# Kernel tuning notes

Measured on AMD Instinct MI355X. Metric: run time of the kernel, lower is better.

## Reference

```python
import jax, jax.numpy as jnp
import numpy as np

B, N, C = 4, 2048, 768
H = 12
DH = C // H
HID = int(C * 4.0)
SCALE = DH ** -0.5
EPS = 1e-5


def layernorm(x, g, b):
    mu = jnp.mean(x, axis=-1, keepdims=True)
    var = jnp.var(x, axis=-1, keepdims=True)
    return (x - mu) * jax.lax.rsqrt(var + EPS) * g + b


def setup_inputs() -> dict:
    key = jax.random.key(0)
    ks = jax.random.split(key, 10)
    s = lambda fan_in: 1.0 / np.sqrt(fan_in)
    return {
        "x": jax.random.normal(ks[0], (B, N, C), dtype=jnp.float32),
        "ln1_g": jnp.ones((C,), jnp.float32),
        "ln1_b": jnp.zeros((C,), jnp.float32),
        "w_qkv": jax.random.uniform(ks[1], (C, 3 * C), jnp.float32, -s(C), s(C)),
        "w_proj": jax.random.uniform(ks[2], (C, C), jnp.float32, -s(C), s(C)),
        "b_proj": jnp.zeros((C,), jnp.float32),
        "ln2_g": jnp.ones((C,), jnp.float32),
        "ln2_b": jnp.zeros((C,), jnp.float32),
        "w_fc1": jax.random.uniform(ks[3], (C, HID), jnp.float32, -s(C), s(C)),
        "b_fc1": jnp.zeros((HID,), jnp.float32),
        "w_fc2": jax.random.uniform(ks[4], (HID, C), jnp.float32, -s(HID), s(HID)),
        "b_fc2": jnp.zeros((C,), jnp.float32),
    }


def reference(x, ln1_g, ln1_b, w_qkv, w_proj, b_proj, ln2_g, ln2_b, w_fc1, b_fc1, w_fc2, b_fc2):
    # --- attention branch ---
    h = layernorm(x, ln1_g, ln1_b)                       # [B,N,C]
    qkv = (h @ w_qkv).reshape(B, N, 3, H, DH)
    q = qkv[:, :, 0].transpose(0, 2, 1, 3)               # [B,H,N,DH]
    k = qkv[:, :, 1].transpose(0, 2, 1, 3)
    v = qkv[:, :, 2].transpose(0, 2, 1, 3)
    attn = jnp.einsum('bhnd,bhmd->bhnm', q, k) * SCALE   # [B,H,N,N]
    attn = jax.nn.softmax(attn, axis=-1)
    y = jnp.einsum('bhnm,bhmd->bhnd', attn, v)           # [B,H,N,DH]
    y = y.transpose(0, 2, 1, 3).reshape(B, N, C)
    y = y @ w_proj + b_proj
    x = x + y
    # --- MLP branch ---
    h = layernorm(x, ln2_g, ln2_b)
    h = jax.nn.gelu(h @ w_fc1 + b_fc1, approximate=False)
    h = h @ w_fc2 + b_fc2
    return x + h
```

## Files before the change

kernel.cpp:

```cpp
#include <hip/hip_runtime.h>
#include <stdint.h>

#define DEV __device__ __forceinline__

typedef __attribute__((ext_vector_type(8))) short bf16x8;
typedef __attribute__((ext_vector_type(4))) float f32x4;
typedef __attribute__((ext_vector_type(4))) short s16x4;

DEV short f2bf(float f) {
    union { float f; unsigned u; } v; v.f = f;
    unsigned r = v.u + 0x7fffu + ((v.u >> 16) & 1u);
    return (short)(r >> 16);
}

DEV uint32_t cvtpk(float lo, float hi) {
    uint32_t r;
    asm("v_cvt_pk_bf16_f32 %0, %1, %2" : "=v"(r) : "v"(lo), "v"(hi));
    return r;
}

typedef const unsigned int __attribute__((address_space(1)))* gp1;
typedef unsigned int __attribute__((address_space(3)))* lp3;

DEV void gload16(const void* g, void* l) {
    __builtin_amdgcn_global_load_lds((gp1)g, (lp3)l, 16, 0, 0);
}

DEV void wait1_barrier() { asm volatile("s_waitcnt vmcnt(1)\ns_barrier" ::: "memory"); }
DEV void wait0_barrier() { asm volatile("s_waitcnt vmcnt(0)\ns_barrier" ::: "memory"); }

__global__ __launch_bounds__(256) void tcvt4(
    const float* __restrict__ W0, short* __restrict__ T0,
    const float* __restrict__ W1, short* __restrict__ T1,
    const float* __restrict__ W2, short* __restrict__ T2,
    const float* __restrict__ W3, short* __restrict__ T3)
{
    __shared__ float t[32][33];
    int bid = blockIdx.x;
    const float* W; short* WT; int K, N, nx, lb;
    if (bid < 1728)      { W = W0; WT = T0; K = 768;  N = 2304; nx = 72; lb = bid; }
    else if (bid < 2304) { W = W1; WT = T1; K = 768;  N = 768;  nx = 24; lb = bid - 1728; }
    else if (bid < 4608) { W = W2; WT = T2; K = 768;  N = 3072; nx = 96; lb = bid - 2304; }
    else                 { W = W3; WT = T3; K = 3072; N = 768;  nx = 24; lb = bid - 4608; }
    int n0 = (lb % nx) * 32, k0 = (lb / nx) * 32;
    int tx = threadIdx.x & 31, ty = threadIdx.x >> 5;
#pragma unroll
    for (int i = 0; i < 32; i += 8)
        t[ty + i][tx] = W[(size_t)(k0 + ty + i) * N + n0 + tx];
    __syncthreads();
#pragma unroll
    for (int i = 0; i < 32; i += 8)
        WT[(size_t)(n0 + ty + i) * K + k0 + tx] = f2bf(t[tx][ty + i]);
}

__global__ __launch_bounds__(256) void ln_bf16(
    const float* __restrict__ x, const float* __restrict__ gam,
    const float* __restrict__ bet, short* __restrict__ out)
{
    const int w = threadIdx.x >> 6, lane = threadIdx.x & 63;
    const size_t row = (size_t)blockIdx.x * 4 + w;
    const float* xr = x + row * 768;
    float4 v[3];
    float s = 0.f, ss = 0.f;
#pragma unroll
    for (int k = 0; k < 3; ++k) {
        v[k] = *(const float4*)(xr + k * 256 + lane * 4);
        s  += v[k].x + v[k].y + v[k].z + v[k].w;
        ss += v[k].x * v[k].x + v[k].y * v[k].y + v[k].z * v[k].z + v[k].w * v[k].w;
    }
#pragma unroll
    for (int i = 1; i < 64; i <<= 1) { s += __shfl_xor(s, i, 64); ss += __shfl_xor(ss, i, 64); }
    const float inv = 1.f / 768.f;
    float mu = s * inv;
    float var = ss * inv - mu * mu;
    float rstd = rsqrtf(var + 1e-5f);
#pragma unroll
    for (int k = 0; k < 3; ++k) {
        int c = k * 256 + lane * 4;
        float vv[4] = { v[k].x, v[k].y, v[k].z, v[k].w };
        s16x4 o;
#pragma unroll
        for (int j = 0; j < 4; ++j)
            o[j] = f2bf((vv[j] - mu) * rstd * gam[c + j] + bet[c + j]);
        *(s16x4*)(out + row * 768 + c) = o;
    }
}

template<int MODE>
DEV void gemm_body(
    const short* __restrict__ A, const short* __restrict__ Bt,
    int M, int N, int K,
    const float* __restrict__ bias, const float* __restrict__ resid,
    float* __restrict__ outf, short* __restrict__ outb,
    short* __restrict__ qo, short* __restrict__ ko, short* __restrict__ vo,
    char* lds)
{
    const int tid = threadIdx.x;
    const int w = tid >> 6, lane = tid & 63;
    const int g = lane >> 4, l15 = lane & 15;
    const int brow = blockIdx.x * 128, bcol = blockIdx.y * 128;
    const int wr = w >> 2, wc = w & 3;
    f32x4 acc[2][2] = {};

    int aoff[2], boff[2];
#pragma unroll
    for (int m = 0; m < 2; ++m) {
        int ra = wr * 32 + m * 16 + l15;
        aoff[m] = ra * 64 + ((g * 16) ^ (((ra >> 1) & 3) << 4));
    }
#pragma unroll
    for (int n = 0; n < 2; ++n) {
        int rb = wc * 32 + n * 16 + l15;
        boff[n] = 8192 + rb * 64 + ((g * 16) ^ (((rb >> 1) & 3) << 4));
    }
    const int dStage = tid * 16;
    const char* pSrc;
    {
        int r = dStage >> 6, b = dStage & 63;
        int bs = b ^ (((r >> 1) & 3) << 4);
        pSrc = (tid < 512)
             ? (const char*)(A  + (size_t)(brow + r) * K) + bs
             : (const char*)(Bt + (size_t)(bcol + (r - 128)) * K) + bs;
    }

#define GSTAGE(BUF, OFF) gload16(pSrc + (OFF), lds + (BUF) * 16384 + dStage)

    const int KT = K >> 5;
    GSTAGE(0, 0);
    GSTAGE(1, 64);
    wait1_barrier();

    const int NM = KT / 3;
    for (int mi = 0; mi < NM; ++mi) {
#pragma unroll
        for (int u = 0; u < 3; ++u) {
            const int s = mi * 3 + u;
            if (s + 2 < KT) GSTAGE((u + 2) % 3, (u + 2) * 64);
            bf16x8 af[2], bfg[2];
#pragma unroll
            for (int m = 0; m < 2; ++m)
                af[m]  = *(const bf16x8*)(lds + u * 16384 + aoff[m]);
#pragma unroll
            for (int n = 0; n < 2; ++n)
                bfg[n] = *(const bf16x8*)(lds + u * 16384 + boff[n]);
#pragma unroll
            for (int m = 0; m < 2; ++m)
#pragma unroll
                for (int n = 0; n < 2; ++n)
                    acc[m][n] = __builtin_amdgcn_mfma_f32_16x16x32_bf16(af[m], bfg[n], acc[m][n], 0, 0, 0);
            if (s + 1 < KT) {
                if (s + 2 < KT) wait1_barrier();
                else            wait0_barrier();
            }
        }
        pSrc += 192;
    }
#undef GSTAGE

#pragma unroll
    for (int m = 0; m < 2; ++m) {
#pragma unroll
        for (int n = 0; n < 2; ++n) {
#pragma unroll
            for (int j = 0; j < 4; ++j) {
                int r = brow + wr * 32 + m * 16 + g * 4 + j;
                int c = bcol + wc * 32 + n * 16 + l15;
                float v = acc[m][n][j];
                if (MODE == 0) {
                    int which = c / 768, cc = c % 768;
                    int h = cc >> 6, d = cc & 63;
                    int b_ = r >> 11, nn = r & 2047;
                    size_t bh = (size_t)b_ * 12 + h;
                    if (which == 0)      qo[(bh * 2048 + nn) * 64 + d] = f2bf(v * 0.18033688011112042f);
                    else if (which == 1) ko[(bh * 2048 + nn) * 64 + d] = f2bf(v);
                    else                 vo[(bh * 64 + d) * 2048 + nn] = f2bf(v);
                } else if (MODE == 1) {
                    outf[(size_t)r * N + c] = v + bias[c] + resid[(size_t)r * N + c];
                } else {
                    float t = v + bias[c];
                    float ge = 0.5f * t * (1.0f + erff(t * 0.70710678118654752f));
                    outb[(size_t)r * N + c] = f2bf(ge);
                }
            }
        }
    }
}

__global__ __launch_bounds__(1024, 8) void g_qkv(
    const short* A, const short* Bt, int M, int N, int K,
    short* qo, short* ko, short* vo)
{
    __shared__ __align__(16) char lds[49152];
    gemm_body<0>(A, Bt, M, N, K, nullptr, nullptr, nullptr, nullptr, qo, ko, vo, lds);
}
__global__ __launch_bounds__(1024, 8) void g_proj(
    const short* A, const short* Bt, int M, int N, int K,
    const float* bias, const float* resid, float* outf)
{
    __shared__ __align__(16) char lds[49152];
    gemm_body<1>(A, Bt, M, N, K, bias, resid, outf, nullptr, nullptr, nullptr, nullptr, lds);
}
__global__ __launch_bounds__(1024, 8) void g_fc1(
    const short* A, const short* Bt, int M, int N, int K,
    const float* bias, short* outb)
{
    __shared__ __align__(16) char lds[49152];
    gemm_body<2>(A, Bt, M, N, K, bias, nullptr, nullptr, outb, nullptr, nullptr, nullptr, lds);
}
__global__ __launch_bounds__(1024, 8) void g_fc2(
    const short* A, const short* Bt, int M, int N, int K,
    const float* bias, const float* resid, float* outf)
{
    __shared__ __align__(16) char lds[49152];
    gemm_body<1>(A, Bt, M, N, K, bias, resid, outf, nullptr, nullptr, nullptr, nullptr, lds);
}

__global__ __launch_bounds__(256, 3) void attn_fwd(
    const short* __restrict__ Q, const short* __restrict__ Kg,
    const short* __restrict__ Vt, short* __restrict__ Y)
{
    __shared__ __align__(16) char alds[43008];
    const int tid = threadIdx.x, w = tid >> 6, lane = tid & 63;
    const int g = lane >> 4, l15 = lane & 15;
    const int bid = blockIdx.y * gridDim.x + blockIdx.x;
    const int nwg = gridDim.x * gridDim.y;
    const int logical = (bid & 7) * (nwg >> 3) + (bid >> 3);
    const int bh = logical >> 4;
    const int q0 = (logical & 15) * 128 + w * 32;
    const short* Qb = Q  + (size_t)bh * 2048 * 64;
    const short* Kb = Kg + (size_t)bh * 2048 * 64;
    const short* Vb = Vt + (size_t)bh * 64 * 2048;

    bf16x8 qf[2][2];
#pragma unroll
    for (int m = 0; m < 2; ++m)
#pragma unroll
        for (int kk = 0; kk < 2; ++kk)
            qf[m][kk] = *(const bf16x8*)(Qb + (size_t)(q0 + m * 16 + l15) * 64 + kk * 32 + g * 8);

    f32x4 accO[2][4] = {};
    float lpart[2] = { 0.f, 0.f };

    int koff[2][2], voff[4], poff[2], pwoff[2][2];
#pragma unroll
    for (int n = 0; n < 2; ++n) {
        int key = n * 16 + l15;
#pragma unroll
        for (int kk = 0; kk < 2; ++kk)
            koff[kk][n] = key * 128 + ((kk * 64 + g * 16) ^ ((key & 7) << 4));
    }
#pragma unroll
    for (int n = 0; n < 4; ++n) {
        int d = n * 16 + l15;
        voff[n] = 16384 + d * 64 + ((g * 16) ^ (((d >> 1) & 3) << 4));
    }
#pragma unroll
    for (int m = 0; m < 2; ++m) {
        int qr = m * 16 + l15;
        poff[m] = 32768 + w * 2560 + qr * 80 + g * 16;
#pragma unroll
        for (int n = 0; n < 2; ++n)
            pwoff[m][n] = 32768 + w * 2560 + qr * 80 + n * 32 + g * 8;
    }
    int dK, dV; const char* pK3; const char* pV3;
    {
        int bb = w * 1024;
        int L = bb + lane * 16;
        int rk = L >> 7, bk_ = L & 127;
        int bsk = bk_ ^ ((rk & 7) << 4);
        dK = bb;
        pK3 = (const char*)(Kb + (size_t)rk * 64) + bsk;
        int rv = L >> 6, bv = L & 63;
        int bsv = bv ^ (((rv >> 1) & 3) << 4);
        dV = bb;
        pV3 = (const char*)(Vb + (size_t)rv * 2048) + bsv;
    }

#define ASTAGE(SLOT) do { \
    gload16(pK3, alds + dK + (SLOT) * 4096); \
    gload16(pV3, alds + 16384 + dV + (SLOT) * 4096); \
    pK3 += 4096; pV3 += 64; } while (0)

#define ACOMPUTE(SLOT) do { \
    f32x4 s2[2][2] = {}; \
    __builtin_amdgcn_s_setprio(1); \
    _Pragma("unroll") \
    for (int kk = 0; kk < 2; ++kk) { \
        bf16x8 kf[2]; \
        _Pragma("unroll") \
        for (int n = 0; n < 2; ++n) \
            kf[n] = *(const bf16x8*)(alds + (SLOT) * 4096 + koff[kk][n]); \
        _Pragma("unroll") \
        for (int m = 0; m < 2; ++m) \
            _Pragma("unroll") \
            for (int n = 0; n < 2; ++n) \
                s2[m][n] = __builtin_amdgcn_mfma_f32_16x16x32_bf16(kf[n], qf[m][kk], s2[m][n], 0, 0, 0); \
    } \
    __builtin_amdgcn_s_setprio(0); \
    _Pragma("unroll") \
    for (int m = 0; m < 2; ++m) \
        _Pragma("unroll") \
        for (int n = 0; n < 2; ++n) { \
            float e0 = __builtin_amdgcn_exp2f(s2[m][n][0]); \
            float e1 = __builtin_amdgcn_exp2f(s2[m][n][1]); \
            float e2 = __builtin_amdgcn_exp2f(s2[m][n][2]); \
            float e3 = __builtin_amdgcn_exp2f(s2[m][n][3]); \
            lpart[m] += (e0 + e1) + (e2 + e3); \
            uint2 pk; pk.x = cvtpk(e0, e1); pk.y = cvtpk(e2, e3); \
            *(uint2*)(alds + pwoff[m][n]) = pk; \
        } \
    __builtin_amdgcn_s_setprio(1); \
    { \
        bf16x8 vf[4], pf[2]; \
        _Pragma("unroll") \
        for (int n = 0; n < 4; ++n) \
            vf[n] = *(const bf16x8*)(alds + (SLOT) * 4096 + voff[n]); \
        _Pragma("unroll") \
        for (int m = 0; m < 2; ++m) \
            pf[m] = *(const bf16x8*)(alds + poff[m]); \
        _Pragma("unroll") \
        for (int m = 0; m < 2; ++m) \
            _Pragma("unroll") \
            for (int n = 0; n < 4; ++n) \
                accO[m][n] = __builtin_amdgcn_mfma_f32_16x16x32_bf16(pf[m], vf[n], accO[m][n], 0, 0, 0); \
    } \
    __builtin_amdgcn_s_setprio(0); } while (0)

    ASTAGE(0);
    ASTAGE(1);
    wait0_barrier();

    for (int om = 0; om < 15; ++om) {
        ASTAGE(2); ACOMPUTE(0); ASTAGE(3); ACOMPUTE(1); wait0_barrier();
        ASTAGE(0); ACOMPUTE(2); ASTAGE(1); ACOMPUTE(3); wait0_barrier();
    }
    ASTAGE(2); ACOMPUTE(0); ASTAGE(3); ACOMPUTE(1); wait0_barrier();
    ACOMPUTE(2); ACOMPUTE(3);

#undef ASTAGE
#undef ACOMPUTE

#pragma unroll
    for (int m = 0; m < 2; ++m) {
        lpart[m] += __shfl_xor(lpart[m], 16, 64);
        lpart[m] += __shfl_xor(lpart[m], 32, 64);
    }

    int b_ = bh / 12, h = bh % 12;
#pragma unroll
    for (int m = 0; m < 2; ++m) {
        float linv[4];
#pragma unroll
        for (int j = 0; j < 4; ++j)
            linv[j] = 1.0f / __shfl(lpart[m], g * 4 + j, 64);
#pragma unroll
        for (int n = 0; n < 4; ++n)
#pragma unroll
            for (int j = 0; j < 4; ++j) {
                int qq = q0 + m * 16 + g * 4 + j;
                int d = n * 16 + l15;
                Y[((size_t)b_ * 2048 + qq) * 768 + h * 64 + d] = f2bf(accO[m][n][j] * linv[j]);
            }
    }
}

extern "C" void kernel_launch(void* const* d_in, const int* in_sizes, int n_in,
                              void* d_out, int out_size, void* d_ws, size_t ws_size,
                              hipStream_t stream)
{
    const float* x      = (const float*)d_in[0];
    const float* ln1_g  = (const float*)d_in[1];
    const float* ln1_b  = (const float*)d_in[2];
    const float* w_qkv  = (const float*)d_in[3];
    const float* w_proj = (const float*)d_in[4];
    const float* b_proj = (const float*)d_in[5];
    const float* ln2_g  = (const float*)d_in[6];
    const float* ln2_b  = (const float*)d_in[7];
    const float* w_fc1  = (const float*)d_in[8];
    const float* b_fc1  = (const float*)d_in[9];
    const float* w_fc2  = (const float*)d_in[10];
    const float* b_fc2  = (const float*)d_in[11];

    char* ws = (char*)d_ws;
    size_t off = 0;
    auto alloc = [&](size_t bytes) -> void* {
        void* p = ws + off; off += (bytes + 255) & ~(size_t)255; return p;
    };
    short* wqkvT = (short*)alloc((size_t)2304 * 768 * 2);
    short* wprojT= (short*)alloc((size_t)768 * 768 * 2);
    short* wfc1T = (short*)alloc((size_t)3072 * 768 * 2);
    short* wfc2T = (short*)alloc((size_t)768 * 3072 * 2);
    short* h1    = (short*)alloc((size_t)8192 * 768 * 2);
    short* qb    = (short*)alloc((size_t)48 * 2048 * 64 * 2);
    short* kb    = (short*)alloc((size_t)48 * 2048 * 64 * 2);
    short* vtb   = (short*)alloc((size_t)48 * 64 * 2048 * 2);
    short* yb    = (short*)alloc((size_t)8192 * 768 * 2);
    float* X1    = (float*)alloc((size_t)8192 * 768 * 4);
    short* h2    = (short*)alloc((size_t)8192 * 768 * 2);
    short* h3    = (short*)alloc((size_t)8192 * 3072 * 2);

    tcvt4<<<6912, 256, 0, stream>>>(w_qkv, wqkvT, w_proj, wprojT,
                                    w_fc1, wfc1T, w_fc2, wfc2T);

    ln_bf16<<<2048, 256, 0, stream>>>(x, ln1_g, ln1_b, h1);

    g_qkv<<<dim3(64, 18), 1024, 0, stream>>>(h1, wqkvT, 8192, 2304, 768, qb, kb, vtb);

    attn_fwd<<<dim3(16, 48), 256, 0, stream>>>(qb, kb, vtb, yb);

    g_proj<<<dim3(64, 6), 1024, 0, stream>>>(yb, wprojT, 8192, 768, 768, b_proj, x, X1);

    ln_bf16<<<2048, 256, 0, stream>>>(X1, ln2_g, ln2_b, h2);

    g_fc1<<<dim3(64, 24), 1024, 0, stream>>>(h2, wfc1T, 8192, 3072, 768, b_fc1, h3);

    g_fc2<<<dim3(64, 6), 1024, 0, stream>>>(h3, wfc2T, 8192, 768, 3072, b_fc2, X1, (float*)d_out);
}
```

Measured before the change: 262.6 us.

## Use 256x128 tiles with 4x4 MFMA per wave for QKV and FC1 GEMMs

Adds a larger-tile GEMM body for the QKV and FC1 projections: 512 threads per block, 256x128 output tile, each wave computing a 64x64 sub-tile with 16 MFMAs per K step. Staging drops from a three-buffer scheme to two LDS buffers with a full wait per step. The aim is more register-level reuse of LDS fragments and fewer global loads per FLOP. The cost is higher register pressure, less load/compute overlap from the simpler double buffering, and fewer blocks in flight.

Result: slower. 943.4 us (+259.3%).

```diff
diff --git a/kernel.cpp b/kernel.cpp
--- a/kernel.cpp
+++ b/kernel.cpp
@@ -87,84 +87,76 @@
 }
 
 template<int MODE>
-DEV void gemm_body(
+DEV void gemm_body_big(
     const short* __restrict__ A, const short* __restrict__ Bt,
     int M, int N, int K,
-    const float* __restrict__ bias, const float* __restrict__ resid,
-    float* __restrict__ outf, short* __restrict__ outb,
+    const float* __restrict__ bias, short* __restrict__ outb,
     short* __restrict__ qo, short* __restrict__ ko, short* __restrict__ vo,
     char* lds)
 {
     const int tid = threadIdx.x;
     const int w = tid >> 6, lane = tid & 63;
     const int g = lane >> 4, l15 = lane & 15;
-    const int brow = blockIdx.x * 128, bcol = blockIdx.y * 128;
-    const int wr = w >> 2, wc = w & 3;
-    f32x4 acc[2][2] = {};
-
-    int aoff[2], boff[2];
-#pragma unroll
-    for (int m = 0; m < 2; ++m) {
-        int ra = wr * 32 + m * 16 + l15;
+    const int brow = blockIdx.x * 256, bcol = blockIdx.y * 128;
+    const int wr = w >> 1, wc = w & 1;
+    f32x4 acc[4][4] = {};
+
+    int aoff[4], boff[4];
+#pragma unroll
+    for (int m = 0; m < 4; ++m) {
+        int ra = wr * 64 + m * 16 + l15;
         aoff[m] = ra * 64 + ((g * 16) ^ (((ra >> 1) & 3) << 4));
-    }
-#pragma unroll
-    for (int n = 0; n < 2; ++n) {
-        int rb = wc * 32 + n * 16 + l15;
-        boff[n] = 8192 + rb * 64 + ((g * 16) ^ (((rb >> 1) & 3) << 4));
-    }
-    const int dStage = tid * 16;
-    const char* pSrc;
-    {
-        int r = dStage >> 6, b = dStage & 63;
-        int bs = b ^ (((r >> 1) & 3) << 4);
-        pSrc = (tid < 512)
-             ? (const char*)(A  + (size_t)(brow + r) * K) + bs
-             : (const char*)(Bt + (size_t)(bcol + (r - 128)) * K) + bs;
-    }
-
-#define GSTAGE(BUF, OFF) gload16(pSrc + (OFF), lds + (BUF) * 16384 + dStage)
+        int rb = wc * 64 + m * 16 + l15;
+        boff[m] = 16384 + rb * 64 + ((g * 16) ^ (((rb >> 1) & 3) << 4));
+    }
+    const int L = tid * 16;
+    const int r0 = L >> 6, bb = L & 63;
+    const int bs = bb ^ (((r0 >> 1) & 3) << 4);
+    const char* pA0 = (const char*)(A  + (size_t)(brow + r0) * K) + bs;
+    const char* pA1 = (const char*)(A  + (size_t)(brow + 128 + r0) * K) + bs;
+    const char* pB  = (const char*)(Bt + (size_t)(bcol + r0) * K) + bs;
+    const int dA0 = L, dA1 = 8192 + L, dB = 16384 + L;
+
+#define GSTAGE(BUF, OFF) do { \
+    gload16(pA0 + (OFF), lds + (BUF) * 24576 + dA0); \
+    gload16(pA1 + (OFF), lds + (BUF) * 24576 + dA1); \
+    gload16(pB  + (OFF), lds + (BUF) * 24576 + dB); } while (0)
+
+#define COMPUTE(BUF) do { \
+    bf16x8 af[4], bfg[4]; \
+    _Pragma("unroll") \
+    for (int m = 0; m < 4; ++m) { \
+        af[m]  = *(const bf16x8*)(lds + (BUF) * 24576 + aoff[m]); \
+        bfg[m] = *(const bf16x8*)(lds + (BUF) * 24576 + boff[m]); \
+    } \
+    _Pragma("unroll") \
+    for (int m = 0; m < 4; ++m) \
+        _Pragma("unroll") \
+        for (int n = 0; n < 4; ++n) \
+            acc[m][n] = __builtin_amdgcn_mfma_f32_16x16x32_bf16(af[m], bfg[n], acc[m][n], 0, 0, 0); \
+    } while (0)
 
     const int KT = K >> 5;
     GSTAGE(0, 0);
-    GSTAGE(1, 64);
-    wait1_barrier();
-
-    const int NM = KT / 3;
-    for (int mi = 0; mi < NM; ++mi) {
-#pragma unroll
-        for (int u = 0; u < 3; ++u) {
-            const int s = mi * 3 + u;
-            if (s + 2 < KT) GSTAGE((u + 2) % 3, (u + 2) * 64);
-            bf16x8 af[2], bfg[2];
-#pragma unroll
-            for (int m = 0; m < 2; ++m)
-                af[m]  = *(const bf16x8*)(lds + u * 16384 + aoff[m]);
-#pragma unroll
-            for (int n = 0; n < 2; ++n)
-                bfg[n] = *(const bf16x8*)(lds + u * 16384 + boff[n]);
-#pragma unroll
-            for (int m = 0; m < 2; ++m)
-#pragma unroll
-                for (int n = 0; n < 2; ++n)
-                    acc[m][n] = __builtin_amdgcn_mfma_f32_16x16x32_bf16(af[m], bfg[n], acc[m][n], 0, 0, 0);
-            if (s + 1 < KT) {
-                if (s + 2 < KT) wait1_barrier();
-                else            wait0_barrier();
-            }
-        }
-        pSrc += 192;
-    }
+    wait0_barrier();
+    for (int mi = 0; mi < KT / 2 - 1; ++mi) {
+        GSTAGE(1, 64);  COMPUTE(0); wait0_barrier();
+        GSTAGE(0, 128); COMPUTE(1); wait0_barrier();
+        pA0 += 128; pA1 += 128; pB += 128;
+    }
+    GSTAGE(1, 64); COMPUTE(0); wait0_barrier();
+    COMPUTE(1);
 #undef GSTAGE
-
-#pragma unroll
-    for (int m = 0; m < 2; ++m) {
-#pragma unroll
-        for (int n = 0; n < 2; ++n) {
+#undef COMPUTE
+
+#pragma unroll
+    for (int m = 0; m < 4; ++m) {
+#pragma unroll
+        for (int n = 0; n < 4; ++n) {
 #pragma unroll
             for (int j = 0; j < 4; ++j) {
-                int r = brow + wr * 32 + m * 16 + g * 4 + j;
-                int c = bcol + wc * 32 + n * 16 + l15;
+                int r = brow + wr * 64 + m * 16 + g * 4 + j;
+                int c = bcol + wc * 64 + n * 16 + l15;
                 float v = acc[m][n][j];
                 if (MODE == 0) {
                     int which = c / 768, cc = c % 768;
@@ -174,8 +166,6 @@
                     if (which == 0)      qo[(bh * 2048 + nn) * 64 + d] = f2bf(v * 0.18033688011112042f);
                     else if (which == 1) ko[(bh * 2048 + nn) * 64 + d] = f2bf(v);
                     else                 vo[(bh * 64 + d) * 2048 + nn] = f2bf(v);
-                } else if (MODE == 1) {
-                    outf[(size_t)r * N + c] = v + bias[c] + resid[(size_t)r * N + c];
                 } else {
                     float t = v + bias[c];
                     float ge = 0.5f * t * (1.0f + erff(t * 0.70710678118654752f));
@@ -186,33 +176,115 @@
     }
 }
 
-__global__ __launch_bounds__(1024, 8) void g_qkv(
+__global__ __launch_bounds__(512, 6) void gb_qkv(
     const short* A, const short* Bt, int M, int N, int K,
     short* qo, short* ko, short* vo)
 {
     __shared__ __align__(16) char lds[49152];
-    gemm_body<0>(A, Bt, M, N, K, nullptr, nullptr, nullptr, nullptr, qo, ko, vo, lds);
-}
+    gemm_body_big<0>(A, Bt, M, N, K, nullptr, nullptr, qo, ko, vo, lds);
+}
+__global__ __launch_bounds__(512, 6) void gb_fc1(
+    const short* A, const short* Bt, int M, int N, int K,
+    const float* bias, short* outb)
+{
+    __shared__ __align__(16) char lds[49152];
+    gemm_body_big<2>(A, Bt, M, N, K, bias, outb, nullptr, nullptr, nullptr, lds);
+}
+
+template<int MODE>
+DEV void gemm_body(
+    const short* __restrict__ A, const short* __restrict__ Bt,
+    int M, int N, int K,
+    const float* __restrict__ bias, const float* __restrict__ resid,
+    float* __restrict__ outf, char* lds)
+{
+    const int tid = threadIdx.x;
+    const int w = tid >> 6, lane = tid & 63;
+    const int g = lane >> 4, l15 = lane & 15;
+    const int brow = blockIdx.x * 128, bcol = blockIdx.y * 128;
+    const int wr = w >> 2, wc = w & 3;
+    f32x4 acc[2][2] = {};
+
+    int aoff[2], boff[2];
+#pragma unroll
+    for (int m = 0; m < 2; ++m) {
+        int ra = wr * 32 + m * 16 + l15;
+        aoff[m] = ra * 64 + ((g * 16) ^ (((ra >> 1) & 3) << 4));
+    }
+#pragma unroll
+    for (int n = 0; n < 2; ++n) {
+        int rb = wc * 32 + n * 16 + l15;
+        boff[n] = 8192 + rb * 64 + ((g * 16) ^ (((rb >> 1) & 3) << 4));
+    }
+    const int dStage = tid * 16;
+    const char* pSrc;
+    {
+        int r = dStage >> 6, b = dStage & 63;
+        int bs = b ^ (((r >> 1) & 3) << 4);
+        pSrc = (tid < 512)
+             ? (const char*)(A  + (size_t)(brow + r) * K) + bs
+             : (const char*)(Bt + (size_t)(bcol + (r - 128)) * K) + bs;
+    }
+
+#define GSTAGE(BUF, OFF) gload16(pSrc + (OFF), lds + (BUF) * 16384 + dStage)
+
+    const int KT = K >> 5;
+    GSTAGE(0, 0);
+    GSTAGE(1, 64);
+    wait1_barrier();
+
+    const int NM = KT / 3;
+    for (int mi = 0; mi < NM; ++mi) {
+#pragma unroll
+        for (int u = 0; u < 3; ++u) {
+            const int s = mi * 3 + u;
+            if (s + 2 < KT) GSTAGE((u + 2) % 3, (u + 2) * 64);
+            bf16x8 af[2], bfg[2];
+#pragma unroll
+            for (int m = 0; m < 2; ++m)
+                af[m]  = *(const bf16x8*)(lds + u * 16384 + aoff[m]);
+#pragma unroll
+            for (int n = 0; n < 2; ++n)
+                bfg[n] = *(const bf16x8*)(lds + u * 16384 + boff[n]);
+#pragma unroll
+            for (int m = 0; m < 2; ++m)
+#pragma unroll
+                for (int n = 0; n < 2; ++n)
+                    acc[m][n] = __builtin_amdgcn_mfma_f32_16x16x32_bf16(af[m], bfg[n], acc[m][n], 0, 0, 0);
+            if (s + 1 < KT) {
+                if (s + 2 < KT) wait1_barrier();
+                else            wait0_barrier();
+            }
+        }
+        pSrc += 192;
+    }
+#undef GSTAGE
+
+#pragma unroll
+    for (int m = 0; m < 2; ++m)
+#pragma unroll
+        for (int n = 0; n < 2; ++n)
+#pragma unroll
+            for (int j = 0; j < 4; ++j) {
+                int r = brow + wr * 32 + m * 16 + g * 4 + j;
+                int c = bcol + wc * 32 + n * 16 + l15;
+                outf[(size_t)r * N + c] = acc[m][n][j] + bias[c] + resid[(size_t)r * N + c];
+            }
+}
+
 __global__ __launch_bounds__(1024, 8) void g_proj(
     const short* A, const short* Bt, int M, int N, int K,
     const float* bias, const float* resid, float* outf)
 {
     __shared__ __align__(16) char lds[49152];
-    gemm_body<1>(A, Bt, M, N, K, bias, resid, outf, nullptr, nullptr, nullptr, nullptr, lds);
-}
-__global__ __launch_bounds__(1024, 8) void g_fc1(
-    const short* A, const short* Bt, int M, int N, int K,
-    const float* bias, short* outb)
-{
-    __shared__ __align__(16) char lds[49152];
-    gemm_body<2>(A, Bt, M, N, K, bias, nullptr, nullptr, outb, nullptr, nullptr, nullptr, lds);
+    gemm_body<1>(A, Bt, M, N, K, bias, resid, outf, lds);
 }
 __global__ __launch_bounds__(1024, 8) void g_fc2(
     const short* A, const short* Bt, int M, int N, int K,
     const float* bias, const float* resid, float* outf)
 {
     __shared__ __align__(16) char lds[49152];
-    gemm_body<1>(A, Bt, M, N, K, bias, resid, outf, nullptr, nullptr, nullptr, nullptr, lds);
+    gemm_body<1>(A, Bt, M, N, K, bias, resid, outf, lds);
 }
 
 __global__ __launch_bounds__(256, 3) void attn_fwd(
@@ -404,7 +476,7 @@
 
     ln_bf16<<<2048, 256, 0, stream>>>(x, ln1_g, ln1_b, h1);
 
-    g_qkv<<<dim3(64, 18), 1024, 0, stream>>>(h1, wqkvT, 8192, 2304, 768, qb, kb, vtb);
+    gb_qkv<<<dim3(32, 18), 512, 0, stream>>>(h1, wqkvT, 8192, 2304, 768, qb, kb, vtb);
 
     attn_fwd<<<dim3(16, 48), 256, 0, stream>>>(qb, kb, vtb, yb);
 
@@ -412,7 +484,7 @@
 
     ln_bf16<<<2048, 256, 0, stream>>>(X1, ln2_g, ln2_b, h2);
 
-    g_fc1<<<dim3(64, 24), 1024, 0, stream>>>(h2, wfc1T, 8192, 3072, 768, b_fc1, h3);
+    gb_fc1<<<dim3(32, 24), 512, 0, stream>>>(h2, wfc1T, 8192, 3072, 768, b_fc1, h3);
 
     g_fc2<<<dim3(64, 6), 1024, 0, stream>>>(h3, wfc2T, 8192, 768, 3072, b_fc2, X1, (float*)d_out);
 }
```
